# Performance work log

Measured on AMD Instinct MI355X. Metric: run time of the kernel, lower is better.

## Reference

```python
import jax, jax.numpy as jnp
import numpy as np

N_NODES = 25000
N_EDGES = 400000
N_GRAPHS = 1000
HID = 185
IN_CH = 9
EPS = 1e-5  # BatchNorm eps (eval mode: uses running stats)


def setup_inputs() -> dict:
    key = jax.random.key(0)
    ks = jax.random.split(key, 12)
    x = jax.random.normal(ks[0], (N_NODES, IN_CH), jnp.float32)
    edge_index = jax.random.randint(ks[1], (2, N_EDGES), 0, N_NODES, jnp.int32)
    batch = jnp.sort(jax.random.randint(ks[2], (N_NODES,), 0, N_GRAPHS, jnp.int32))
    W0 = jax.random.normal(ks[3], (IN_CH, HID), jnp.float32) * 0.3
    b0 = jnp.zeros((HID,), jnp.float32)
    W_h = jax.random.normal(ks[4], (3, HID, HID), jnp.float32) * 0.07
    b_h = jnp.zeros((3, HID), jnp.float32)
    bn_gamma = 1.0 + 0.1 * jax.random.normal(ks[5], (4, HID), jnp.float32)
    bn_beta = 0.1 * jax.random.normal(ks[6], (4, HID), jnp.float32)
    bn_mean = 0.1 * jax.random.normal(ks[7], (4, HID), jnp.float32)
    bn_var = jax.random.uniform(ks[8], (4, HID), jnp.float32, 0.5, 1.5)
    W_jk = jax.random.normal(ks[9], (4 * HID, HID), jnp.float32) * 0.05
    b_jk = jnp.zeros((HID,), jnp.float32)
    W_out = jax.random.normal(ks[10], (HID, 1), jnp.float32) * 0.1
    b_out = jnp.zeros((1,), jnp.float32)
    return dict(x=x, edge_index=edge_index, batch=batch, W0=W0, b0=b0,
                W_h=W_h, b_h=b_h, bn_gamma=bn_gamma, bn_beta=bn_beta,
                bn_mean=bn_mean, bn_var=bn_var, W_jk=W_jk, b_jk=b_jk,
                W_out=W_out, b_out=b_out)


def reference(x, edge_index, batch, W0, b0, W_h, b_h, bn_gamma, bn_beta,
              bn_mean, bn_var, W_jk, b_jk, W_out, b_out):
    N = x.shape[0]
    # GCN normalization with self-loops (gcn_norm, edge_weight = 1)
    loop = jnp.arange(N, dtype=edge_index.dtype)
    src = jnp.concatenate([edge_index[0], loop])  # [E+N]
    dst = jnp.concatenate([edge_index[1], loop])  # [E+N]
    deg = jax.ops.segment_sum(jnp.ones_like(dst, dtype=x.dtype), dst, num_segments=N)
    dis = jnp.where(deg > 0, jax.lax.rsqrt(jnp.maximum(deg, 1.0)), 0.0)
    enorm = dis[src] * dis[dst]  # [E+N]

    def gcn_conv(h, W, b):
        h = h @ W                                   # [N, HID]
        msg = h[src] * enorm[:, None]               # gather + scale, [E+N, HID]
        return jax.ops.segment_sum(msg, dst, num_segments=N) + b

    def bn_relu(h, i):
        h = (h - bn_mean[i]) * jax.lax.rsqrt(bn_var[i] + EPS) * bn_gamma[i] + bn_beta[i]
        return jax.nn.relu(h)  # dropout is identity in eval mode

    xs = []
    h = bn_relu(gcn_conv(x, W0, b0), 0)
    xs.append(h)
    for i in range(3):
        h = bn_relu(gcn_conv(h, W_h[i], b_h[i]), i + 1)
        xs.append(h)
    # JumpingKnowledge 'cat' + internal lin (740 -> 185)
    h = jnp.concatenate(xs, axis=-1) @ W_jk + b_jk  # [N, HID]
    # global_max_pool over graphs
    pooled = jax.ops.segment_max(h, batch, num_segments=N_GRAPHS)  # [G, HID]
    return pooled @ W_out + b_out  # [G, 1]
```

## Files before the change

### kernel.cpp

```cpp
#include <hip/hip_runtime.h>
#include <hip/hip_bf16.h>

#define N_NODES 25000
#define N_EDGES 400000
#define N_GRAPHS 1000
#define HID 185
#define EPS 1e-5f
#define XPITCH 768
#define APITCH 36

typedef __attribute__((ext_vector_type(8))) short bf16x8;
typedef __attribute__((ext_vector_type(4))) float f32x4;

__device__ __forceinline__ short f2bf(float f) {
    union { float f; unsigned u; } v; v.f = f;
    unsigned r = v.u + 0x7FFFu + ((v.u >> 16) & 1u);
    return (short)(r >> 16);
}
__device__ __forceinline__ float bfl(unsigned u) { return __uint_as_float(u << 16); }
__device__ __forceinline__ float bfh(unsigned u) { return __uint_as_float(u & 0xFFFF0000u); }
__device__ __forceinline__ unsigned pk2(float lo, float hi) {
    return (unsigned)(unsigned short)f2bf(lo) | ((unsigned)(unsigned short)f2bf(hi) << 16);
}

#define HW (3 * 192 * 192)
#define JW (192 * 768)
#define CNTPAD 25024
__global__ void k_setup(const float* __restrict__ W_h, const float* __restrict__ W_jk,
                        const float* __restrict__ b0, const float* __restrict__ b_h,
                        const float* __restrict__ gamma, const float* __restrict__ beta,
                        const float* __restrict__ mean, const float* __restrict__ var,
                        int* __restrict__ cnt,
                        short* __restrict__ Wt_h, short* __restrict__ Wt_jk,
                        float* __restrict__ bnsc, float* __restrict__ bnsh) {
    int idx = blockIdx.x * 256 + threadIdx.x;
    if (idx < CNTPAD) { cnt[idx] = 0; return; }
    int p = idx - CNTPAD;
    if (p < HW) {
        int l = p / (192 * 192);
        int r = p % (192 * 192);
        int n = r / 192, k = r % 192;
        float v = (n < HID && k < HID) ? W_h[(l * HID + k) * HID + n] : 0.0f;
        Wt_h[p] = f2bf(v);
    } else if (p < HW + JW) {
        int j2 = p - HW;
        int n = j2 / 768, kk = j2 % 768;
        int l = kk / 192, j = kk % 192;
        float v = (n < HID && j < HID) ? W_jk[(l * HID + j) * HID + n] : 0.0f;
        Wt_jk[j2] = f2bf(v);
    } else if (p < HW + JW + 4 * 192) {
        int li = p - HW - JW;
        int l = li / 192, c = li % 192;
        float sc = 0.0f, sh = 0.0f;
        if (c < HID) {
            float bb = (l == 0) ? b0[c] : b_h[(l - 1) * HID + c];
            sc = rsqrtf(var[l * HID + c] + EPS) * gamma[l * HID + c];
            sh = (bb - mean[l * HID + c]) * sc + beta[l * HID + c];
        }
        bnsc[li] = sc;
        bnsh[li] = sh;
    }
}

__global__ void k_deg(const int* __restrict__ dst, int* cnt, int E) {
    int i = blockIdx.x * blockDim.x + threadIdx.x;
    if (i < E) atomicAdd(&cnt[dst[i]], 1);
}

__global__ __launch_bounds__(256) void k_scan_part(const int* __restrict__ cnt,
                                                   int* __restrict__ bsum,
                                                   float* __restrict__ dis, int N) {
    int i = blockIdx.x * 256 + threadIdx.x;
    int v = (i < N) ? cnt[i] : 0;
    if (i < N) dis[i] = rsqrtf((float)(v + 1));
    #pragma unroll
    for (int off = 32; off; off >>= 1) v += __shfl_down(v, off);
    __shared__ int s[4];
    if ((threadIdx.x & 63) == 0) s[threadIdx.x >> 6] = v;
    __syncthreads();
    if (threadIdx.x == 0) bsum[blockIdx.x] = s[0] + s[1] + s[2] + s[3];
}

__global__ __launch_bounds__(256) void k_scan_add(const int* __restrict__ cnt,
                                                  const int* __restrict__ bsum,
                                                  int* __restrict__ rowptr, int N) {
    __shared__ int s[256];
    const int t = threadIdx.x;
    const int b = blockIdx.x;
    int partial = 0;
    for (int i = t; i < b; i += 256) partial += bsum[i];
    s[t] = partial; __syncthreads();
    for (int off = 128; off; off >>= 1) {
        if (t < off) s[t] += s[t + off];
        __syncthreads();
    }
    const int base = s[0];
    __syncthreads();
    int i = b * 256 + t;
    int v = (i < N) ? cnt[i] : 0;
    s[t] = v; __syncthreads();
    for (int off = 1; off < 256; off <<= 1) {
        int x2 = (t >= off) ? s[t - off] : 0;
        __syncthreads();
        s[t] += x2;
        __syncthreads();
    }
    if (i < N) rowptr[i] = base + s[t] - v;
}

__global__ void k_scatter(const int* __restrict__ src, const int* __restrict__ dst,
                          const float* __restrict__ dis,
                          int* rowptr, int2* __restrict__ csr, int E) {
    int e = blockIdx.x * blockDim.x + threadIdx.x;
    if (e < E) {
        int d = dst[e];
        int s = src[e];
        int o = atomicAdd(&rowptr[d], 1);
        csr[o] = make_int2(s, __float_as_int(dis[s]));
    }
}

__global__ void k_aggr0(const float* __restrict__ x, const float* __restrict__ dis,
                        const int* __restrict__ rowptr, const int2* __restrict__ csr,
                        float* __restrict__ xa, int N) {
    int idx = blockIdx.x * blockDim.x + threadIdx.x;
    int n = idx >> 4;
    int c = idx & 15;
    if (n >= N || c >= 9) return;
    float dn = dis[n];
    float acc = x[n * 9 + c] * dn;
    int end = rowptr[n];
    int e = n ? rowptr[n - 1] : 0;
    for (; e + 4 <= end; e += 4) {
        int2 p0 = csr[e], p1 = csr[e + 1], p2 = csr[e + 2], p3 = csr[e + 3];
        acc += x[p0.x * 9 + c] * __int_as_float(p0.y)
             + x[p1.x * 9 + c] * __int_as_float(p1.y)
             + x[p2.x * 9 + c] * __int_as_float(p2.y)
             + x[p3.x * 9 + c] * __int_as_float(p3.y);
    }
    for (; e < end; ++e) {
        int2 p = csr[e];
        acc += x[p.x * 9 + c] * __int_as_float(p.y);
    }
    xa[n * 9 + c] = acc * dn;
}

__global__ __launch_bounds__(192) void k_gemm0(const float* __restrict__ A,
                                               const float* __restrict__ W,
                                               const float* __restrict__ bnsc,
                                               const float* __restrict__ bnsh,
                                               short* __restrict__ xcat, int N) {
    __shared__ float As[8 * 9];
    const int tid = threadIdx.x;
    const int r0 = blockIdx.x * 8;
    for (int idx = tid; idx < 72; idx += 192) {
        int r = idx & 7, k = idx >> 3;
        int row = r0 + r;
        As[idx] = (row < N) ? A[row * 9 + k] : 0.0f;
    }
    __syncthreads();
    const int c = tid;
    float res[8];
    #pragma unroll
    for (int r = 0; r < 8; ++r) res[r] = 0.0f;
    if (c < HID) {
        float acc[8] = {0,0,0,0,0,0,0,0};
        for (int k = 0; k < 9; ++k) {
            float w = W[k * HID + c];
            #pragma unroll
            for (int r = 0; r < 8; ++r) acc[r] += As[k * 8 + r] * w;
        }
        float sc = bnsc[c], sh = bnsh[c];
        #pragma unroll
        for (int r = 0; r < 8; ++r)
            res[r] = fmaxf(acc[r] * sc + sh, 0.0f);
    }
    #pragma unroll
    for (int r = 0; r < 8; ++r) {
        int row = r0 + r;
        if (row < N) xcat[row * XPITCH + c] = (c < HID) ? f2bf(res[r]) : (short)0;
    }
}

template<int KCH>
__global__ __launch_bounds__(256) void k_mgemm(const short* __restrict__ A,
                                               const short* __restrict__ Bt,
                                               short* __restrict__ Cout, int N) {
    __shared__ short As[64 * APITCH];
    __shared__ short Bs[192 * APITCH];
    const int tid = threadIdx.x;
    const int wave = tid >> 6;
    const int lane = tid & 63;
    const int quad = lane >> 4;
    const int lm = lane & 15;
    const int r0 = blockIdx.x * 64;
    const int KTOT = KCH * 32;
    const int arow = tid >> 2, aseg = tid & 3;

    f32x4 acc[4][3];
    #pragma unroll
    for (int i = 0; i < 4; ++i)
        #pragma unroll
        for (int j = 0; j < 3; ++j) acc[i][j] = (f32x4){0.f, 0.f, 0.f, 0.f};

    for (int kc = 0; kc < KCH; ++kc) {
        const int k0 = kc * 32;
        {
            int grow = r0 + arow;
            bf16x8 v = (bf16x8){0,0,0,0,0,0,0,0};
            if (grow < N) v = *(const bf16x8*)(A + grow * XPITCH + k0 + aseg * 8);
            *(bf16x8*)(As + arow * APITCH + aseg * 8) = v;
        }
        #pragma unroll
        for (int i = 0; i < 3; ++i) {
            int u = tid + i * 256;
            int n = u >> 2, seg = u & 3;
            bf16x8 v = *(const bf16x8*)(Bt + n * KTOT + k0 + seg * 8);
            *(bf16x8*)(Bs + n * APITCH + seg * 8) = v;
        }
        __syncthreads();
        bf16x8 a[4], b[3];
        #pragma unroll
        for (int mt = 0; mt < 4; ++mt)
            a[mt] = *(const bf16x8*)(As + (mt * 16 + lm) * APITCH + quad * 8);
        #pragma unroll
        for (int nt = 0; nt < 3; ++nt)
            b[nt] = *(const bf16x8*)(Bs + (wave * 48 + nt * 16 + lm) * APITCH + quad * 8);
        #pragma unroll
        for (int mt = 0; mt < 4; ++mt)
            #pragma unroll
            for (int nt = 0; nt < 3; ++nt)
                acc[mt][nt] = __builtin_amdgcn_mfma_f32_16x16x32_bf16(a[mt], b[nt], acc[mt][nt], 0, 0, 0);
        __syncthreads();
    }
    #pragma unroll
    for (int mt = 0; mt < 4; ++mt) {
        #pragma unroll
        for (int nt = 0; nt < 3; ++nt) {
            int col = wave * 48 + nt * 16 + lm;
            #pragma unroll
            for (int r = 0; r < 4; ++r) {
                int row = r0 + mt * 16 + quad * 4 + r;
                if (row < N) Cout[row * 192 + col] = f2bf(acc[mt][nt][r]);
            }
        }
    }
}

__global__ __launch_bounds__(256) void k_aggr_bn(const short* __restrict__ tmp16,
                                                 const float* __restrict__ dis,
                                                 const int* __restrict__ rowptr,
                                                 const int2* __restrict__ csr,
                                                 const float* __restrict__ bnsc,
                                                 const float* __restrict__ bnsh,
                                                 short* __restrict__ outp, int N) {
    int n = (blockIdx.x << 2) + (threadIdx.x >> 6);
    if (n >= N) return;
    int lane = threadIdx.x & 63;
    int c0 = (lane < 48) ? (lane << 2) : 0;
    float dn = dis[n];
    float a0, a1, a2, a3;
    {
        uint2 v = *(const uint2*)(tmp16 + (size_t)n * 192 + c0);
        a0 = bfl(v.x) * dn; a1 = bfh(v.x) * dn; a2 = bfl(v.y) * dn; a3 = bfh(v.y) * dn;
    }
    int end = rowptr[n];
    int e = n ? rowptr[n - 1] : 0;
    for (; e + 4 <= end; e += 4) {
        int2 p0 = csr[e], p1 = csr[e + 1], p2 = csr[e + 2], p3 = csr[e + 3];
        float w0 = __int_as_float(p0.y), w1 = __int_as_float(p1.y);
        float w2 = __int_as_float(p2.y), w3 = __int_as_float(p3.y);
        uint2 v0 = *(const uint2*)(tmp16 + (size_t)p0.x * 192 + c0);
        uint2 v1 = *(const uint2*)(tmp16 + (size_t)p1.x * 192 + c0);
        uint2 v2 = *(const uint2*)(tmp16 + (size_t)p2.x * 192 + c0);
        uint2 v3 = *(const uint2*)(tmp16 + (size_t)p3.x * 192 + c0);
        a0 += bfl(v0.x) * w0; a1 += bfh(v0.x) * w0; a2 += bfl(v0.y) * w0; a3 += bfh(v0.y) * w0;
        a0 += bfl(v1.x) * w1; a1 += bfh(v1.x) * w1; a2 += bfl(v1.y) * w1; a3 += bfh(v1.y) * w1;
        a0 += bfl(v2.x) * w2; a1 += bfh(v2.x) * w2; a2 += bfl(v2.y) * w2; a3 += bfh(v2.y) * w2;
        a0 += bfl(v3.x) * w3; a1 += bfh(v3.x) * w3; a2 += bfl(v3.y) * w3; a3 += bfh(v3.y) * w3;
    }
    for (; e < end; ++e) {
        int2 p = csr[e];
        float w = __int_as_float(p.y);
        uint2 v = *(const uint2*)(tmp16 + (size_t)p.x * 192 + c0);
        a0 += bfl(v.x) * w; a1 += bfh(v.x) * w; a2 += bfl(v.y) * w; a3 += bfh(v.y) * w;
    }
    float4 sc = *(const float4*)(bnsc + c0);
    float4 sh = *(const float4*)(bnsh + c0);
    float o0 = fmaxf(a0 * dn * sc.x + sh.x, 0.0f);
    float o1 = fmaxf(a1 * dn * sc.y + sh.y, 0.0f);
    float o2 = fmaxf(a2 * dn * sc.z + sh.z, 0.0f);
    float o3 = fmaxf(a3 * dn * sc.w + sh.w, 0.0f);
    if (lane < 48) {
        uint2 p;
        p.x = pk2(o0, o1);
        p.y = pk2(o2, o3);
        *(uint2*)(outp + (size_t)n * XPITCH + c0) = p;
    }
}

__global__ __launch_bounds__(192) void k_pool_out(const short* __restrict__ jk,
                                                  const int* __restrict__ batch,
                                                  const float* __restrict__ b_jk,
                                                  const float* __restrict__ W_out,
                                                  const float* __restrict__ b_out,
                                                  float* __restrict__ out, int N) {
    __shared__ int bounds[2];
    __shared__ float partial[3];
    const int g = blockIdx.x;
    const int tid = threadIdx.x;
    if (tid < 2) {
        int key = g + tid;
        int lo = 0, hi = N;
        while (lo < hi) {
            int mid = (lo + hi) >> 1;
            if (batch[mid] < key) lo = mid + 1; else hi = mid;
        }
        bounds[tid] = lo;
    }
    __syncthreads();
    const int beg = bounds[0], end = bounds[1];
    float mx = -3.4e38f;
    for (int n = beg; n < end; ++n)
        mx = fmaxf(mx, bfl((unsigned)(unsigned short)jk[(size_t)n * 192 + tid]));
    float p = (tid < HID) ? (mx + b_jk[tid]) * W_out[tid] : 0.0f;
    #pragma unroll
    for (int off = 32; off; off >>= 1) p += __shfl_down(p, off);
    if ((tid & 63) == 0) partial[tid >> 6] = p;
    __syncthreads();
    if (tid == 0) out[g] = partial[0] + partial[1] + partial[2] + b_out[0];
}

extern "C" void kernel_launch(void* const* d_in, const int* in_sizes, int n_in,
                              void* d_out, int out_size, void* d_ws, size_t ws_size,
                              hipStream_t stream) {
    const float* x      = (const float*)d_in[0];
    const int*   ei     = (const int*)  d_in[1];
    const int*   batch  = (const int*)  d_in[2];
    const float* W0     = (const float*)d_in[3];
    const float* b0     = (const float*)d_in[4];
    const float* W_h    = (const float*)d_in[5];
    const float* b_h    = (const float*)d_in[6];
    const float* gamma  = (const float*)d_in[7];
    const float* beta   = (const float*)d_in[8];
    const float* mean   = (const float*)d_in[9];
    const float* var    = (const float*)d_in[10];
    const float* W_jk   = (const float*)d_in[11];
    const float* b_jk   = (const float*)d_in[12];
    const float* W_out  = (const float*)d_in[13];
    const float* b_out  = (const float*)d_in[14];
    float* out = (float*)d_out;

    const int N = N_NODES, E = N_EDGES, G = N_GRAPHS;
    const int NB = (N + 255) / 256;

    float* dis   = (float*)d_ws;
    float* xa    = dis + 25024;
    float* bnsc  = xa + 225024;
    float* bnsh  = bnsc + 768;
    int2*  csr   = (int2*)(bnsh + 768);
    short* xcat  = (short*)(csr + 400000);
    short* tmp16 = xcat + 19200000;
    short* Wt_h  = tmp16 + 4800000;
    short* Wt_jk = Wt_h + 110592;
    int* rowptr  = (int*)(Wt_jk + 147456);
    int* cnt     = rowptr + 25024;
    int* bsum    = cnt + 25024;

    const int* src = ei;
    const int* dst = ei + E;

    k_setup<<<(CNTPAD + HW + JW + 4 * 192 + 255) / 256, 256, 0, stream>>>(
        W_h, W_jk, b0, b_h, gamma, beta, mean, var, cnt, Wt_h, Wt_jk, bnsc, bnsh);
    k_deg<<<(E + 255) / 256, 256, 0, stream>>>(dst, cnt, E);
    k_scan_part<<<NB, 256, 0, stream>>>(cnt, bsum, dis, N);
    k_scan_add<<<NB, 256, 0, stream>>>(cnt, bsum, rowptr, N);
    k_scatter<<<(E + 255) / 256, 256, 0, stream>>>(src, dst, dis, rowptr, csr, E);

    k_aggr0<<<(N * 16 + 255) / 256, 256, 0, stream>>>(x, dis, rowptr, csr, xa, N);
    k_gemm0<<<(N + 7) / 8, 192, 0, stream>>>(xa, W0, bnsc, bnsh, xcat, N);

    const int MB = (N + 63) / 64;
    for (int l = 1; l < 4; ++l) {
        k_mgemm<6><<<MB, 256, 0, stream>>>(xcat + (l - 1) * 192,
                                           Wt_h + (l - 1) * 192 * 192, tmp16, N);
        k_aggr_bn<<<(N + 3) / 4, 256, 0, stream>>>(tmp16, dis, rowptr, csr,
                                                   bnsc + l * 192, bnsh + l * 192,
                                                   xcat + l * 192, N);
    }

    k_mgemm<24><<<MB, 256, 0, stream>>>(xcat, Wt_jk, tmp16, N);

    k_pool_out<<<G, 192, 0, stream>>>(tmp16, batch, b_jk, W_out, b_out, out, N);
}
```

Before: 305.4 us.

## Aggregate before GEMM, fuse BN+ReLU into GEMM epilogue, merge scan kernels

Each hidden GCN layer now does the sparse neighbour aggregation first (A·h) and the dense transform second ((A·h)·W), using associativity, with BatchNorm and ReLU applied in the MFMA GEMM epilogue. The aggregation uses 192-thread blocks, so no lanes sit idle as they did in the old 64-lane-per-node layout. The two-pass prefix scan becomes a single kernel where each block re-sums all preceding counts directly, which removes one launch but adds redundant reads for later blocks. The GEMM result is now rounded to bf16 after aggregation rather than before, which shifts where precision is lost.

```diff
diff --git a/kernel.cpp b/kernel.cpp
--- a/kernel.cpp
+++ b/kernel.cpp
@@ -67,28 +67,14 @@
     if (i < E) atomicAdd(&cnt[dst[i]], 1);
 }
 
-__global__ __launch_bounds__(256) void k_scan_part(const int* __restrict__ cnt,
-                                                   int* __restrict__ bsum,
-                                                   float* __restrict__ dis, int N) {
-    int i = blockIdx.x * 256 + threadIdx.x;
-    int v = (i < N) ? cnt[i] : 0;
-    if (i < N) dis[i] = rsqrtf((float)(v + 1));
-    #pragma unroll
-    for (int off = 32; off; off >>= 1) v += __shfl_down(v, off);
-    __shared__ int s[4];
-    if ((threadIdx.x & 63) == 0) s[threadIdx.x >> 6] = v;
-    __syncthreads();
-    if (threadIdx.x == 0) bsum[blockIdx.x] = s[0] + s[1] + s[2] + s[3];
-}
-
-__global__ __launch_bounds__(256) void k_scan_add(const int* __restrict__ cnt,
-                                                  const int* __restrict__ bsum,
-                                                  int* __restrict__ rowptr, int N) {
+__global__ __launch_bounds__(256) void k_scan(const int* __restrict__ cnt,
+                                              int* __restrict__ rowptr,
+                                              float* __restrict__ dis, int N) {
     __shared__ int s[256];
     const int t = threadIdx.x;
     const int b = blockIdx.x;
     int partial = 0;
-    for (int i = t; i < b; i += 256) partial += bsum[i];
+    for (int i = t; i < b * 256; i += 256) partial += cnt[i];
     s[t] = partial; __syncthreads();
     for (int off = 128; off; off >>= 1) {
         if (t < off) s[t] += s[t + off];
@@ -98,6 +84,7 @@
     __syncthreads();
     int i = b * 256 + t;
     int v = (i < N) ? cnt[i] : 0;
+    if (i < N) dis[i] = rsqrtf((float)(v + 1));
     s[t] = v; __syncthreads();
     for (int off = 1; off < 256; off <<= 1) {
         int x2 = (t >= off) ? s[t - off] : 0;
@@ -182,10 +169,54 @@
     }
 }
 
-template<int KCH>
-__global__ __launch_bounds__(256) void k_mgemm(const short* __restrict__ A,
+__global__ __launch_bounds__(192) void k_aggr(const short* __restrict__ feat, int fpitch,
+                                              const float* __restrict__ dis,
+                                              const int* __restrict__ rowptr,
+                                              const int2* __restrict__ csr,
+                                              short* __restrict__ outp, int N) {
+    const int t = threadIdx.x;
+    const int n = blockIdx.x * 4 + t / 48;
+    const int c0 = (t % 48) * 4;
+    if (n >= N) return;
+    float dn = dis[n];
+    float a0, a1, a2, a3;
+    {
+        uint2 v = *(const uint2*)(feat + (size_t)n * fpitch + c0);
+        a0 = bfl(v.x) * dn; a1 = bfh(v.x) * dn; a2 = bfl(v.y) * dn; a3 = bfh(v.y) * dn;
+    }
+    int end = rowptr[n];
+    int e = n ? rowptr[n - 1] : 0;
+    for (; e + 4 <= end; e += 4) {
+        int2 p0 = csr[e], p1 = csr[e + 1], p2 = csr[e + 2], p3 = csr[e + 3];
+        float w0 = __int_as_float(p0.y), w1 = __int_as_float(p1.y);
+        float w2 = __int_as_float(p2.y), w3 = __int_as_float(p3.y);
+        uint2 v0 = *(const uint2*)(feat + (size_t)p0.x * fpitch + c0);
+        uint2 v1 = *(const uint2*)(feat + (size_t)p1.x * fpitch + c0);
+        uint2 v2 = *(const uint2*)(feat + (size_t)p2.x * fpitch + c0);
+        uint2 v3 = *(const uint2*)(feat + (size_t)p3.x * fpitch + c0);
+        a0 += bfl(v0.x) * w0; a1 += bfh(v0.x) * w0; a2 += bfl(v0.y) * w0; a3 += bfh(v0.y) * w0;
+        a0 += bfl(v1.x) * w1; a1 += bfh(v1.x) * w1; a2 += bfl(v1.y) * w1; a3 += bfh(v1.y) * w1;
+        a0 += bfl(v2.x) * w2; a1 += bfh(v2.x) * w2; a2 += bfl(v2.y) * w2; a3 += bfh(v2.y) * w2;
+        a0 += bfl(v3.x) * w3; a1 += bfh(v3.x) * w3; a2 += bfl(v3.y) * w3; a3 += bfh(v3.y) * w3;
+    }
+    for (; e < end; ++e) {
+        int2 p = csr[e];
+        float w = __int_as_float(p.y);
+        uint2 v = *(const uint2*)(feat + (size_t)p.x * fpitch + c0);
+        a0 += bfl(v.x) * w; a1 += bfh(v.x) * w; a2 += bfl(v.y) * w; a3 += bfh(v.y) * w;
+    }
+    uint2 p;
+    p.x = pk2(a0 * dn, a1 * dn);
+    p.y = pk2(a2 * dn, a3 * dn);
+    *(uint2*)(outp + (size_t)n * 192 + c0) = p;
+}
+
+template<int KCH, bool BNOUT>
+__global__ __launch_bounds__(256) void k_mgemm(const short* __restrict__ A, int apitch,
                                                const short* __restrict__ Bt,
-                                               short* __restrict__ Cout, int N) {
+                                               const float* __restrict__ bnsc,
+                                               const float* __restrict__ bnsh,
+                                               short* __restrict__ Cout, int cpitch, int N) {
     __shared__ short As[64 * APITCH];
     __shared__ short Bs[192 * APITCH];
     const int tid = threadIdx.x;
@@ -208,7 +239,7 @@
         {
             int grow = r0 + arow;
             bf16x8 v = (bf16x8){0,0,0,0,0,0,0,0};
-            if (grow < N) v = *(const bf16x8*)(A + grow * XPITCH + k0 + aseg * 8);
+            if (grow < N) v = *(const bf16x8*)(A + (size_t)grow * apitch + k0 + aseg * 8);
             *(bf16x8*)(As + arow * APITCH + aseg * 8) = v;
         }
         #pragma unroll
@@ -234,68 +265,22 @@
         __syncthreads();
     }
     #pragma unroll
-    for (int mt = 0; mt < 4; ++mt) {
-        #pragma unroll
-        for (int nt = 0; nt < 3; ++nt) {
-            int col = wave * 48 + nt * 16 + lm;
+    for (int nt = 0; nt < 3; ++nt) {
+        int col = wave * 48 + nt * 16 + lm;
+        float sc = 1.0f, sh = 0.0f;
+        if (BNOUT) { sc = bnsc[col]; sh = bnsh[col]; }
+        #pragma unroll
+        for (int mt = 0; mt < 4; ++mt) {
             #pragma unroll
             for (int r = 0; r < 4; ++r) {
                 int row = r0 + mt * 16 + quad * 4 + r;
-                if (row < N) Cout[row * 192 + col] = f2bf(acc[mt][nt][r]);
+                if (row < N) {
+                    float v = acc[mt][nt][r];
+                    if (BNOUT) v = fmaxf(v * sc + sh, 0.0f);
+                    Cout[(size_t)row * cpitch + col] = f2bf(v);
+                }
             }
         }
-    }
-}
-
-__global__ __launch_bounds__(256) void k_aggr_bn(const short* __restrict__ tmp16,
-                                                 const float* __restrict__ dis,
-                                                 const int* __restrict__ rowptr,
-                                                 const int2* __restrict__ csr,
-                                                 const float* __restrict__ bnsc,
-                                                 const float* __restrict__ bnsh,
-                                                 short* __restrict__ outp, int N) {
-    int n = (blockIdx.x << 2) + (threadIdx.x >> 6);
-    if (n >= N) return;
-    int lane = threadIdx.x & 63;
-    int c0 = (lane < 48) ? (lane << 2) : 0;
-    float dn = dis[n];
-    float a0, a1, a2, a3;
-    {
-        uint2 v = *(const uint2*)(tmp16 + (size_t)n * 192 + c0);
-        a0 = bfl(v.x) * dn; a1 = bfh(v.x) * dn; a2 = bfl(v.y) * dn; a3 = bfh(v.y) * dn;
-    }
-    int end = rowptr[n];
-    int e = n ? rowptr[n - 1] : 0;
-    for (; e + 4 <= end; e += 4) {
-        int2 p0 = csr[e], p1 = csr[e + 1], p2 = csr[e + 2], p3 = csr[e + 3];
-        float w0 = __int_as_float(p0.y), w1 = __int_as_float(p1.y);
-        float w2 = __int_as_float(p2.y), w3 = __int_as_float(p3.y);
-        uint2 v0 = *(const uint2*)(tmp16 + (size_t)p0.x * 192 + c0);
-        uint2 v1 = *(const uint2*)(tmp16 + (size_t)p1.x * 192 + c0);
-        uint2 v2 = *(const uint2*)(tmp16 + (size_t)p2.x * 192 + c0);
-        uint2 v3 = *(const uint2*)(tmp16 + (size_t)p3.x * 192 + c0);
-        a0 += bfl(v0.x) * w0; a1 += bfh(v0.x) * w0; a2 += bfl(v0.y) * w0; a3 += bfh(v0.y) * w0;
-        a0 += bfl(v1.x) * w1; a1 += bfh(v1.x) * w1; a2 += bfl(v1.y) * w1; a3 += bfh(v1.y) * w1;
-        a0 += bfl(v2.x) * w2; a1 += bfh(v2.x) * w2; a2 += bfl(v2.y) * w2; a3 += bfh(v2.y) * w2;
-        a0 += bfl(v3.x) * w3; a1 += bfh(v3.x) * w3; a2 += bfl(v3.y) * w3; a3 += bfh(v3.y) * w3;
-    }
-    for (; e < end; ++e) {
-        int2 p = csr[e];
-        float w = __int_as_float(p.y);
-        uint2 v = *(const uint2*)(tmp16 + (size_t)p.x * 192 + c0);
-        a0 += bfl(v.x) * w; a1 += bfh(v.x) * w; a2 += bfl(v.y) * w; a3 += bfh(v.y) * w;
-    }
-    float4 sc = *(const float4*)(bnsc + c0);
-    float4 sh = *(const float4*)(bnsh + c0);
-    float o0 = fmaxf(a0 * dn * sc.x + sh.x, 0.0f);
-    float o1 = fmaxf(a1 * dn * sc.y + sh.y, 0.0f);
-    float o2 = fmaxf(a2 * dn * sc.z + sh.z, 0.0f);
-    float o3 = fmaxf(a3 * dn * sc.w + sh.w, 0.0f);
-    if (lane < 48) {
-        uint2 p;
-        p.x = pk2(o0, o1);
-        p.y = pk2(o2, o3);
-        *(uint2*)(outp + (size_t)n * XPITCH + c0) = p;
     }
 }
 
@@ -365,7 +350,6 @@
     short* Wt_jk = Wt_h + 110592;
     int* rowptr  = (int*)(Wt_jk + 147456);
     int* cnt     = rowptr + 25024;
-    int* bsum    = cnt + 25024;
 
     const int* src = ei;
     const int* dst = ei + E;
@@ -373,8 +357,7 @@
     k_setup<<<(CNTPAD + HW + JW + 4 * 192 + 255) / 256, 256, 0, stream>>>(
         W_h, W_jk, b0, b_h, gamma, beta, mean, var, cnt, Wt_h, Wt_jk, bnsc, bnsh);
     k_deg<<<(E + 255) / 256, 256, 0, stream>>>(dst, cnt, E);
-    k_scan_part<<<NB, 256, 0, stream>>>(cnt, bsum, dis, N);
-    k_scan_add<<<NB, 256, 0, stream>>>(cnt, bsum, rowptr, N);
+    k_scan<<<NB, 256, 0, stream>>>(cnt, rowptr, dis, N);
     k_scatter<<<(E + 255) / 256, 256, 0, stream>>>(src, dst, dis, rowptr, csr, E);
 
     k_aggr0<<<(N * 16 + 255) / 256, 256, 0, stream>>>(x, dis, rowptr, csr, xa, N);
@@ -382,14 +365,16 @@
 
     const int MB = (N + 63) / 64;
     for (int l = 1; l < 4; ++l) {
-        k_mgemm<6><<<MB, 256, 0, stream>>>(xcat + (l - 1) * 192,
-                                           Wt_h + (l - 1) * 192 * 192, tmp16, N);
-        k_aggr_bn<<<(N + 3) / 4, 256, 0, stream>>>(tmp16, dis, rowptr, csr,
-                                                   bnsc + l * 192, bnsh + l * 192,
-                                                   xcat + l * 192, N);
-    }
-
-    k_mgemm<24><<<MB, 256, 0, stream>>>(xcat, Wt_jk, tmp16, N);
+        k_aggr<<<(N + 3) / 4, 192, 0, stream>>>(xcat + (l - 1) * 192, XPITCH,
+                                                dis, rowptr, csr, tmp16, N);
+        k_mgemm<6, true><<<MB, 256, 0, stream>>>(tmp16, 192,
+                                                 Wt_h + (l - 1) * 192 * 192,
+                                                 bnsc + l * 192, bnsh + l * 192,
+                                                 xcat + l * 192, XPITCH, N);
+    }
+
+    k_mgemm<24, false><<<MB, 256, 0, stream>>>(xcat, XPITCH, Wt_jk,
+                                               nullptr, nullptr, tmp16, 192, N);
 
     k_pool_out<<<G, 192, 0, stream>>>(tmp16, batch, b_jk, W_out, b_out, out, N);
 }
```

Result: slower. 313.8 us (+2.7%).
